# Kernel optimization log

Hardware: AMD Instinct MI355X
Metric: run time of the kernel (lower is better)

Reference implementation:

```python
import jax, jax.numpy as jnp
import numpy as np

B, S, D, H, DH, L, FF = 1, 4096, 768, 12, 64, 12, 3072
V, P = 50265, 4098
BLK = 256          # block size for banded attention
W_ONE = 256        # one-sided window (attention_window=512)
EPS = 1e-5


def layernorm(x, g, b):
    mu = jnp.mean(x, axis=-1, keepdims=True)
    var = jnp.mean((x - mu) ** 2, axis=-1, keepdims=True)
    return (x - mu) * jax.lax.rsqrt(var + EPS) * g + b


def sliding_attn(q, k, v, mask):
    # q,k,v: [B,H,S,DH]; mask: [B,S] (1=keep). Band |i-j| <= W_ONE.
    nb = S // BLK
    scale = 1.0 / np.sqrt(DH)
    qb = (q * scale).reshape(B, H, nb, BLK, DH)
    kp = jnp.pad(k, ((0, 0), (0, 0), (BLK, BLK), (0, 0))).reshape(B, H, nb + 2, BLK, DH)
    vp = jnp.pad(v, ((0, 0), (0, 0), (BLK, BLK), (0, 0))).reshape(B, H, nb + 2, BLK, DH)
    # each query block attends to key blocks [b-1, b, b+1] -> 3*BLK keys
    kb = jnp.concatenate([kp[:, :, :-2], kp[:, :, 1:-1], kp[:, :, 2:]], axis=3)
    vb = jnp.concatenate([vp[:, :, :-2], vp[:, :, 1:-1], vp[:, :, 2:]], axis=3)
    scores = jnp.einsum('bhnqd,bhnkd->bhnqk', qb, kb)  # [B,H,nb,BLK,3BLK]
    p = jnp.arange(BLK)[:, None]
    o = jnp.arange(3 * BLK)[None, :]
    rel = o - BLK - p
    band = (rel >= -W_ONE) & (rel <= W_ONE)            # [BLK,3BLK]
    mp = jnp.pad(mask.astype(bool), ((0, 0), (BLK, BLK))).reshape(B, nb + 2, BLK)
    mb = jnp.concatenate([mp[:, :-2], mp[:, 1:-1], mp[:, 2:]], axis=2)  # [B,nb,3BLK]
    valid = band[None, None, None, :, :] & mb[:, None, :, None, :]
    scores = jnp.where(valid, scores, jnp.asarray(-1e9, scores.dtype))
    probs = jax.nn.softmax(scores, axis=-1)
    out = jnp.einsum('bhnqk,bhnkd->bhnqd', probs, vb)
    return out.reshape(B, H, S, DH)


def setup_inputs() -> dict:
    keys = iter(jax.random.split(jax.random.key(0), 64))
    rn = lambda shape, s=0.02: jax.random.normal(next(keys), shape, jnp.float32) * s
    inp = {
        'input_ids': jax.random.randint(next(keys), (B, S), 0, V, jnp.int32),
        'attention_mask': jnp.ones((B, S), jnp.int32),
        'emb_word': rn((V, D)), 'emb_pos': rn((P, D)), 'emb_type': rn((1, D)),
        'emb_ln_g': jnp.ones((D,)), 'emb_ln_b': jnp.zeros((D,)),
        'Wq': rn((L, D, D)), 'bq': jnp.zeros((L, D)),
        'Wk': rn((L, D, D)), 'bk': jnp.zeros((L, D)),
        'Wv': rn((L, D, D)), 'bv': jnp.zeros((L, D)),
        'Wo': rn((L, D, D)), 'bo': jnp.zeros((L, D)),
        'ln1_g': jnp.ones((L, D)), 'ln1_b': jnp.zeros((L, D)),
        'W1': rn((L, D, FF)), 'b1': jnp.zeros((L, FF)),
        'W2': rn((L, FF, D)), 'b2': jnp.zeros((L, D)),
        'ln2_g': jnp.ones((L, D)), 'ln2_b': jnp.zeros((L, D)),
        'cW1': rn((D, 512)), 'cb1': jnp.zeros((512,)),
        'cW2': rn((512, 5)), 'cb2': jnp.zeros((5,)),
        'dW1': rn((D, 512)), 'db1': jnp.zeros((512,)),
        'dW2': rn((512, 10)), 'db2': jnp.zeros((10,)),
    }
    return inp


def reference(input_ids, attention_mask, emb_word, emb_pos, emb_type, emb_ln_g, emb_ln_b,
              Wq, bq, Wk, bk, Wv, bv, Wo, bo, ln1_g, ln1_b, W1, b1, W2, b2, ln2_g, ln2_b,
              cW1, cb1, cW2, cb2, dW1, db1, dW2, db2):
    mask = attention_mask
    # RoBERTa-style position ids (pad_token_id=1 offset)
    pos_ids = jnp.cumsum(mask, axis=1) * mask + 1
    x = emb_word[input_ids] + emb_pos[pos_ids] + emb_type[0]
    x = layernorm(x, emb_ln_g, emb_ln_b)
    for i in range(L):
        q = (x @ Wq[i] + bq[i]).reshape(B, S, H, DH).transpose(0, 2, 1, 3)
        k = (x @ Wk[i] + bk[i]).reshape(B, S, H, DH).transpose(0, 2, 1, 3)
        v = (x @ Wv[i] + bv[i]).reshape(B, S, H, DH).transpose(0, 2, 1, 3)
        a = sliding_attn(q, k, v, mask).transpose(0, 2, 1, 3).reshape(B, S, D)
        x = layernorm(x + a @ Wo[i] + bo[i], ln1_g[i], ln1_b[i])
        h = jax.nn.gelu(x @ W1[i] + b1[i], approximate=False)
        x = layernorm(x + h @ W2[i] + b2[i], ln2_g[i], ln2_b[i])
    pooled = x[:, 0, :]
    century = jax.nn.relu(pooled @ cW1 + cb1) @ cW2 + cb2
    decade = jax.nn.relu(pooled @ dW1 + db1) @ dW2 + db2
    return (century, decade)
```

## Files before the change

kernel.cpp:

```cpp
#include <hip/hip_runtime.h>
#include <hip/hip_bf16.h>
#include <math.h>

typedef __bf16 bf16_t;
typedef __bf16 bf16x8 __attribute__((ext_vector_type(8)));
typedef __bf16 bf16x4 __attribute__((ext_vector_type(4)));
typedef float  f32x4  __attribute__((ext_vector_type(4)));
typedef short  s16x4  __attribute__((ext_vector_type(4)));

#define S_LEN 4096
#define DMODEL 768
#define NHEAD 12
#define NLAYER 12
#define FFDIM 3072

static __device__ inline f32x4 mfma16x16x16(bf16x4 a, bf16x4 b, f32x4 c) {
#if __has_builtin(__builtin_amdgcn_mfma_f32_16x16x16_bf16)
  return __builtin_amdgcn_mfma_f32_16x16x16_bf16(a, b, c, 0, 0, 0);
#else
  return __builtin_amdgcn_mfma_f32_16x16x16bf16_1k(
      __builtin_bit_cast(s16x4, a), __builtin_bit_cast(s16x4, b), c, 0, 0, 0);
#endif
}

static __device__ inline void gload_lds16(const void* g, void* l) {
  __builtin_amdgcn_global_load_lds(
      (const __attribute__((address_space(1))) void*)g,
      (__attribute__((address_space(3))) void*)l, 16, 0, 0);
}

__global__ __launch_bounds__(256) void posid_kernel(const int* __restrict__ m,
                                                    int* __restrict__ pids) {
  __shared__ int ps[256];
  int t = threadIdx.x;
  int base = t * 16;
  int loc[16], mv[16];
  int s = 0;
#pragma unroll
  for (int j = 0; j < 16; ++j) { mv[j] = m[base + j]; s += mv[j]; loc[j] = s; }
  ps[t] = s;
  __syncthreads();
  for (int off = 1; off < 256; off <<= 1) {
    int v = (t >= off) ? ps[t - off] : 0;
    __syncthreads();
    ps[t] += v;
    __syncthreads();
  }
  int pre = t ? ps[t - 1] : 0;
#pragma unroll
  for (int j = 0; j < 16; ++j) pids[base + j] = (pre + loc[j]) * mv[j] + 1;
}

__device__ inline float blk_sum(float v, float* sred) {
#pragma unroll
  for (int o = 32; o; o >>= 1) v += __shfl_down(v, o, 64);
  int w = threadIdx.x >> 6;
  __syncthreads();
  if ((threadIdx.x & 63) == 0) sred[w] = v;
  __syncthreads();
  return sred[0] + sred[1] + sred[2] + sred[3];
}

__global__ __launch_bounds__(256) void embed_kernel(
    const int* __restrict__ ids, const int* __restrict__ pids,
    const float* __restrict__ ew, const float* __restrict__ ep,
    const float* __restrict__ et, const float* __restrict__ g,
    const float* __restrict__ b, float* __restrict__ xf,
    bf16_t* __restrict__ xb) {
  __shared__ float sred[4];
  int s = blockIdx.x, t = threadIdx.x;
  long wb = (long)ids[s] * DMODEL;
  long pb = (long)pids[s] * DMODEL;
  float v[3];
#pragma unroll
  for (int j = 0; j < 3; ++j) {
    int d = t + j * 256;
    v[j] = ew[wb + d] + ep[pb + d] + et[d];
  }
  float mu = blk_sum(v[0] + v[1] + v[2], sred) * (1.0f / 768.0f);
  float ss = 0.f;
#pragma unroll
  for (int j = 0; j < 3; ++j) { v[j] -= mu; ss += v[j] * v[j]; }
  float rs = rsqrtf(blk_sum(ss, sred) * (1.0f / 768.0f) + 1e-5f);
#pragma unroll
  for (int j = 0; j < 3; ++j) {
    int d = t + j * 256;
    float o = v[j] * rs * g[d] + b[d];
    xf[(long)s * DMODEL + d] = o;
    xb[(long)s * DMODEL + d] = (bf16_t)o;
  }
}

__global__ __launch_bounds__(256) void ln_kernel(
    const float* __restrict__ in, const float* __restrict__ g,
    const float* __restrict__ b, float* __restrict__ xf,
    bf16_t* __restrict__ xb) {
  __shared__ float sred[4];
  int row = blockIdx.x, t = threadIdx.x;
  const float* r = in + (long)row * DMODEL;
  float v[3] = {r[t], r[t + 256], r[t + 512]};
  float mu = blk_sum(v[0] + v[1] + v[2], sred) * (1.0f / 768.0f);
  float ss = 0.f;
#pragma unroll
  for (int j = 0; j < 3; ++j) { v[j] -= mu; ss += v[j] * v[j]; }
  float rs = rsqrtf(blk_sum(ss, sred) * (1.0f / 768.0f) + 1e-5f);
#pragma unroll
  for (int j = 0; j < 3; ++j) {
    int d = t + j * 256;
    float o = v[j] * rs * g[d] + b[d];
    xf[(long)row * DMODEL + d] = o;
    xb[(long)row * DMODEL + d] = (bf16_t)o;
  }
}

__global__ __launch_bounds__(256) void lnred_kernel(
    const float* __restrict__ pt, int ns, const float* __restrict__ gb,
    const float* __restrict__ g, const float* __restrict__ b,
    float* __restrict__ xf, bf16_t* __restrict__ xb) {
  __shared__ float sred[4];
  const long MN = (long)S_LEN * DMODEL;
  int row = blockIdx.x, t = threadIdx.x;
  long rb = (long)row * DMODEL;
  float v[3];
#pragma unroll
  for (int j = 0; j < 3; ++j) {
    int d = t + j * 256;
    float a = gb[d] + xf[rb + d];
    for (int z = 0; z < ns; ++z) a += pt[(long)z * MN + rb + d];
    v[j] = a;
  }
  float mu = blk_sum(v[0] + v[1] + v[2], sred) * (1.0f / 768.0f);
  float ss = 0.f;
#pragma unroll
  for (int j = 0; j < 3; ++j) { v[j] -= mu; ss += v[j] * v[j]; }
  float rs = rsqrtf(blk_sum(ss, sred) * (1.0f / 768.0f) + 1e-5f);
#pragma unroll
  for (int j = 0; j < 3; ++j) {
    int d = t + j * 256;
    float o = v[j] * rs * g[d] + b[d];
    xf[rb + d] = o;
    xb[rb + d] = (bf16_t)o;
  }
}

__global__ __launch_bounds__(256) void trc_kernel(const float* __restrict__ src,
                                                  bf16_t* __restrict__ dst,
                                                  int R, int C, long srcStride,
                                                  long dstStride) {
  src += (long)blockIdx.z * srcStride;
  dst += (long)blockIdx.z * dstStride;
  __shared__ float tile[64][65];
  int r0 = blockIdx.y * 64, c0 = blockIdx.x * 64;
  int t = threadIdx.x;
  int tr = t >> 4;
  int tc = (t & 15) * 4;
#pragma unroll
  for (int j = 0; j < 4; ++j) {
    int row = tr + j * 16;
    float4 v = *(const float4*)(src + (long)(r0 + row) * C + c0 + tc);
    tile[row][tc] = v.x; tile[row][tc + 1] = v.y;
    tile[row][tc + 2] = v.z; tile[row][tc + 3] = v.w;
  }
  __syncthreads();
#pragma unroll
  for (int j = 0; j < 4; ++j) {
    int row = tr + j * 16;
    bf16x4 v;
    v[0] = (bf16_t)tile[tc + 0][row]; v[1] = (bf16_t)tile[tc + 1][row];
    v[2] = (bf16_t)tile[tc + 2][row]; v[3] = (bf16_t)tile[tc + 3][row];
    *(bf16x4*)(dst + (long)(c0 + row) * R + r0 + tc) = v;
  }
}

__global__ __launch_bounds__(256) void tr_kernel(const bf16_t* __restrict__ src,
                                                 bf16_t* __restrict__ dst,
                                                 int R, int C) {
  __shared__ bf16_t tile[64][68];
  int r0 = blockIdx.y * 64, c0 = blockIdx.x * 64;
  int t = threadIdx.x;
  int tr = t >> 4;
  int tc = (t & 15) * 4;
#pragma unroll
  for (int j = 0; j < 4; ++j) {
    int row = tr + j * 16;
    bf16x4 v = *(const bf16x4*)(src + (long)(r0 + row) * C + c0 + tc);
    tile[row][tc] = v[0]; tile[row][tc + 1] = v[1];
    tile[row][tc + 2] = v[2]; tile[row][tc + 3] = v[3];
  }
  __syncthreads();
#pragma unroll
  for (int j = 0; j < 4; ++j) {
    int row = tr + j * 16;
    bf16x4 v;
    v[0] = tile[tc + 0][row]; v[1] = tile[tc + 1][row];
    v[2] = tile[tc + 2][row]; v[3] = tile[tc + 3][row];
    *(bf16x4*)(dst + (long)(c0 + row) * R + r0 + tc) = v;
  }
}

template <int EP>
__global__ __launch_bounds__(256) void gemm_kernel(
    const bf16_t* __restrict__ A, const bf16_t* __restrict__ Bt, long btStride,
    const float* b0, const float* b1, const float* b2,
    bf16_t* __restrict__ out, long outStride, const float* __restrict__ resf,
    float* __restrict__ tmp, int M, int N, int K, int kc) {
  int z = blockIdx.z;
  const float* bias = nullptr;
  int kBeg = 0;
  if constexpr (EP == 3) {
    kBeg = z * kc;
  } else {
    Bt += (long)z * btStride;
    bias = (z == 0) ? b0 : (z == 1 ? b1 : b2);
    out += (long)z * outStride;
  }

  int nwg = gridDim.x * gridDim.y;
  int bid = blockIdx.y * gridDim.x + blockIdx.x;
  int swz = (bid & 7) * (nwg >> 3) + (bid >> 3);
  int bx = swz % gridDim.x;
  int by = swz / gridDim.x;

  int tid = threadIdx.x;
  int lane = tid & 63;
  int wave = tid >> 6;
  int wm = (wave >> 1) * 64;
  int wn = (wave & 1) * 64;
  int l15 = lane & 15;
  int g4 = lane >> 4;
  int m0 = by * 128;
  int n0 = bx * 128;

  f32x4 acc[4][4] = {};

  __shared__ __align__(16) bf16_t As[128 * 64];
  __shared__ __align__(16) bf16_t Bs[128 * 64];

  for (int kt = kBeg; kt < kBeg + kc; kt += 64) {
#pragma unroll
    for (int c = 0; c < 4; ++c) {
      int L0 = c * 256 + wave * 64;
      int row = (L0 & 127) + lane;
      int gg = L0 >> 7;
      gload_lds16(A + (long)(m0 + row) * K + kt + gg * 8, As + L0 * 8);
      gload_lds16(Bt + (long)(n0 + row) * K + kt + gg * 8, Bs + L0 * 8);
    }
    __syncthreads();
#pragma unroll
    for (int ks = 0; ks < 2; ++ks) {
      bf16x8 af[4], bfr[4];
#pragma unroll
      for (int mt = 0; mt < 4; ++mt)
        af[mt] = *(const bf16x8*)(As + (((ks * 4 + g4) * 128) + wm + mt * 16 + l15) * 8);
#pragma unroll
      for (int nt = 0; nt < 4; ++nt)
        bfr[nt] = *(const bf16x8*)(Bs + (((ks * 4 + g4) * 128) + wn + nt * 16 + l15) * 8);
#pragma unroll
      for (int mt = 0; mt < 4; ++mt)
#pragma unroll
        for (int nt = 0; nt < 4; ++nt)
          acc[mt][nt] = __builtin_amdgcn_mfma_f32_16x16x32_bf16(
              af[mt], bfr[nt], acc[mt][nt], 0, 0, 0);
    }
    __syncthreads();
  }

#pragma unroll
  for (int mt = 0; mt < 4; ++mt)
#pragma unroll
    for (int nt = 0; nt < 4; ++nt) {
      int col = n0 + wn + nt * 16 + l15;
      float bval = (EP == 3) ? 0.f : bias[col];
#pragma unroll
      for (int r = 0; r < 4; ++r) {
        int row = m0 + wm + mt * 16 + g4 * 4 + r;
        float v = acc[mt][nt][r] + bval;
        if (EP == 0) {
          out[(long)row * N + col] = (bf16_t)v;
        } else if (EP == 1) {
          float ge = 0.5f * v * (1.0f + erff(v * 0.70710678118654752f));
          out[(long)row * N + col] = (bf16_t)ge;
        } else if (EP == 2) {
          tmp[(long)row * N + col] = v + resf[(long)row * N + col];
        } else {
          tmp[(long)z * ((long)M * N) + (long)row * N + col] = v;
        }
      }
    }
}

#define NEGM 30000.0f
__global__ __launch_bounds__(64) void attn_kernel(
    const bf16_t* __restrict__ q, const bf16_t* __restrict__ k,
    const bf16_t* __restrict__ vt, bf16_t* __restrict__ outb) {
  int qt = blockIdx.x * 32;
  int hcol = blockIdx.y * 64;
  int lane = threadIdx.x;
  int l15 = lane & 15, g4 = lane >> 4;
  __shared__ __align__(16) float sbuf[32];

  bf16x8 qf[2][2];
#pragma unroll
  for (int nt = 0; nt < 2; ++nt)
#pragma unroll
    for (int ks = 0; ks < 2; ++ks) {
      bf16x8 t = *(const bf16x8*)(q + (long)(qt + nt * 16 + l15) * DMODEL +
                                  hcol + ks * 32 + g4 * 8);
#pragma unroll
      for (int i = 0; i < 8; ++i) t[i] = (bf16_t)((float)t[i] * 0.125f);
      qf[nt][ks] = t;
    }

  f32x4 o[2][4] = {};
  float mS[2], lS[2];
#pragma unroll
  for (int nt = 0; nt < 2; ++nt) { mS[nt] = -NEGM; lS[nt] = 0.f; }

  int kstart = (qt >= 256) ? ((qt - 256) & ~63) : 0;
  int kend = (qt + 288 + 63) & ~63;
  if (kend > S_LEN) kend = S_LEN;

  for (int kb = kstart; kb < kend; kb += 64) {
    bf16x8 kf[4][2];
#pragma unroll
    for (int kt = 0; kt < 4; ++kt)
#pragma unroll
      for (int ks = 0; ks < 2; ++ks)
        kf[kt][ks] = *(const bf16x8*)(k + (long)(kb + kt * 16 + l15) * DMODEL +
                                      hcol + ks * 32 + g4 * 8);
    f32x4 st[4][2] = {};
#pragma unroll
    for (int kt = 0; kt < 4; ++kt)
#pragma unroll
      for (int nt = 0; nt < 2; ++nt) {
        st[kt][nt] = __builtin_amdgcn_mfma_f32_16x16x32_bf16(
            kf[kt][0], qf[nt][0], st[kt][nt], 0, 0, 0);
        st[kt][nt] = __builtin_amdgcn_mfma_f32_16x16x32_bf16(
            kf[kt][1], qf[nt][1], st[kt][nt], 0, 0, 0);
      }
    float alpha[2];
#pragma unroll
    for (int nt = 0; nt < 2; ++nt) {
      int qg = qt + nt * 16 + l15;
      float mx = -NEGM;
#pragma unroll
      for (int kt = 0; kt < 4; ++kt)
#pragma unroll
        for (int r = 0; r < 4; ++r) {
          int kg = kb + kt * 16 + g4 * 4 + r;
          bool valid = (kg >= qg - 256) && (kg <= qg + 256);
          float s = valid ? st[kt][nt][r] : -NEGM;
          st[kt][nt][r] = s;
          mx = fmaxf(mx, s);
        }
      mx = fmaxf(mx, __shfl_xor(mx, 16, 64));
      mx = fmaxf(mx, __shfl_xor(mx, 32, 64));
      float mnew = fmaxf(mS[nt], mx);
      alpha[nt] = exp2f((mS[nt] - mnew) * 1.44269504088896f);
      float ls = 0.f;
#pragma unroll
      for (int kt = 0; kt < 4; ++kt)
#pragma unroll
        for (int r = 0; r < 4; ++r) {
          float p = exp2f((st[kt][nt][r] - mnew) * 1.44269504088896f);
          st[kt][nt][r] = p;
          ls += p;
        }
      ls += __shfl_xor(ls, 16, 64);
      ls += __shfl_xor(ls, 32, 64);
      lS[nt] = lS[nt] * alpha[nt] + ls;
      mS[nt] = mnew;
    }
    if (g4 == 0) {
#pragma unroll
      for (int nt = 0; nt < 2; ++nt) sbuf[nt * 16 + l15] = alpha[nt];
    }
    __syncthreads();
    f32x4 av[2];
#pragma unroll
    for (int qmt = 0; qmt < 2; ++qmt)
      av[qmt] = *(const f32x4*)(sbuf + qmt * 16 + g4 * 4);
#pragma unroll
    for (int qmt = 0; qmt < 2; ++qmt)
#pragma unroll
      for (int dt = 0; dt < 4; ++dt)
#pragma unroll
        for (int r = 0; r < 4; ++r) o[qmt][dt][r] *= av[qmt][r];
#pragma unroll
    for (int kt = 0; kt < 4; ++kt) {
      bf16x4 pa[2];
#pragma unroll
      for (int qmt = 0; qmt < 2; ++qmt)
#pragma unroll
        for (int i = 0; i < 4; ++i) pa[qmt][i] = (bf16_t)st[kt][qmt][i];
      bf16x4 vf[4];
#pragma unroll
      for (int dt = 0; dt < 4; ++dt)
        vf[dt] = *(const bf16x4*)(vt + (long)(hcol + dt * 16 + l15) * S_LEN +
                                  kb + kt * 16 + g4 * 4);
#pragma unroll
      for (int qmt = 0; qmt < 2; ++qmt)
#pragma unroll
        for (int dt = 0; dt < 4; ++dt)
          o[qmt][dt] = mfma16x16x16(pa[qmt], vf[dt], o[qmt][dt]);
    }
    __syncthreads();
  }
  if (g4 == 0) {
#pragma unroll
    for (int nt = 0; nt < 2; ++nt) sbuf[nt * 16 + l15] = lS[nt];
  }
  __syncthreads();
  f32x4 lv[2];
#pragma unroll
  for (int qmt = 0; qmt < 2; ++qmt)
    lv[qmt] = *(const f32x4*)(sbuf + qmt * 16 + g4 * 4);
#pragma unroll
  for (int qmt = 0; qmt < 2; ++qmt)
#pragma unroll
    for (int dt = 0; dt < 4; ++dt)
#pragma unroll
      for (int r = 0; r < 4; ++r)
        outb[(long)(qt + qmt * 16 + g4 * 4 + r) * DMODEL + hcol + dt * 16 +
             l15] = (bf16_t)(o[qmt][dt][r] / lv[qmt][r]);
}

__global__ __launch_bounds__(256) void cls1_kernel(
    const float* __restrict__ xf, const float* cW1, const float* cb1,
    const float* dW1, const float* db1, float* __restrict__ hws) {
  __shared__ float red[4][64];
  bool dec = (blockIdx.y == 1);
  const float* W1 = dec ? dW1 : cW1;
  const float* B1 = dec ? db1 : cb1;
  float* h = hws + (dec ? 512 : 0);
  int t = threadIdx.x;
  int c = (t & 63) + blockIdx.x * 64;
  int ch = t >> 6;
  float s = 0.f;
  for (int k2 = ch * 192; k2 < ch * 192 + 192; ++k2)
    s += xf[k2] * W1[(long)k2 * 512 + c];
  red[ch][t & 63] = s;
  __syncthreads();
  if (t < 64) {
    int col = t + blockIdx.x * 64;
    float a = red[0][t] + red[1][t] + red[2][t] + red[3][t] + B1[col];
    h[col] = fmaxf(a, 0.f);
  }
}

__global__ __launch_bounds__(256) void cls2_kernel(
    const float* __restrict__ hws, const float* cW2, const float* cb2,
    const float* dW2, const float* db2, float* __restrict__ out) {
  __shared__ float sred[4];
  bool dec = (blockIdx.x == 1);
  const float* W2 = dec ? dW2 : cW2;
  const float* B2 = dec ? db2 : cb2;
  const float* h = hws + (dec ? 512 : 0);
  int nout = dec ? 10 : 5;
  float* op = out + (dec ? 5 : 0);
  int t = threadIdx.x;
  float h0 = h[t], h1 = h[t + 256];
  for (int o = 0; o < nout; ++o) {
    float s = h0 * W2[t * nout + o] + h1 * W2[(t + 256) * nout + o];
    float tot = blk_sum(s, sred);
    if (t == 0) op[o] = tot + B2[o];
    __syncthreads();
  }
}

extern "C" void kernel_launch(void* const* d_in, const int* in_sizes, int n_in,
                              void* d_out, int out_size, void* d_ws,
                              size_t ws_size, hipStream_t stream) {
  const int* ids = (const int*)d_in[0];
  const int* amask = (const int*)d_in[1];
  const float* emb_word = (const float*)d_in[2];
  const float* emb_pos = (const float*)d_in[3];
  const float* emb_type = (const float*)d_in[4];
  const float* emb_g = (const float*)d_in[5];
  const float* emb_b = (const float*)d_in[6];
  const float* Wq = (const float*)d_in[7];
  const float* bq = (const float*)d_in[8];
  const float* Wk = (const float*)d_in[9];
  const float* bk = (const float*)d_in[10];
  const float* Wv = (const float*)d_in[11];
  const float* bv = (const float*)d_in[12];
  const float* Wo = (const float*)d_in[13];
  const float* bo = (const float*)d_in[14];
  const float* ln1g = (const float*)d_in[15];
  const float* ln1b = (const float*)d_in[16];
  const float* W1 = (const float*)d_in[17];
  const float* b1 = (const float*)d_in[18];
  const float* W2 = (const float*)d_in[19];
  const float* b2 = (const float*)d_in[20];
  const float* ln2g = (const float*)d_in[21];
  const float* ln2b = (const float*)d_in[22];
  const float* cW1 = (const float*)d_in[23];
  const float* cb1 = (const float*)d_in[24];
  const float* cW2 = (const float*)d_in[25];
  const float* cb2 = (const float*)d_in[26];
  const float* dW1 = (const float*)d_in[27];
  const float* db1 = (const float*)d_in[28];
  const float* dW2 = (const float*)d_in[29];
  const float* db2 = (const float*)d_in[30];
  float* outp = (float*)d_out;

  const size_t SD = (size_t)S_LEN * DMODEL;
  const size_t DD = (size_t)DMODEL * DMODEL;
  const size_t DF = (size_t)DMODEL * FFDIM;
  const size_t SF = (size_t)S_LEN * FFDIM;

  char* p = (char*)d_ws;
  auto carve = [&](size_t bytes) {
    char* r = p;
    p += (bytes + 255) & ~(size_t)255;
    return (void*)r;
  };

  size_t actsBytes = SD * 2 + SD * 4 + 3 * SD * 2 + SD * 2 + SD * 2 + SF * 2 +
                     SD * 4 + S_LEN * 4 + 16 * 256;
  size_t fullW = (36 * DD + 12 * DD + 24 * DF) * 2 + 16 * 256;
  bool full = ws_size >= actsBytes + fullW;

  bf16_t *qkvt, *wot, *w1t, *w2t;
  if (full) {
    qkvt = (bf16_t*)carve(36 * DD * 2);
    wot = (bf16_t*)carve(12 * DD * 2);
    w1t = (bf16_t*)carve(12 * DF * 2);
    w2t = (bf16_t*)carve(12 * DF * 2);
  } else {
    qkvt = (bf16_t*)carve(3 * DD * 2);
    wot = (bf16_t*)carve(DD * 2);
    w1t = (bf16_t*)carve(DF * 2);
    w2t = (bf16_t*)carve(DF * 2);
  }
  bf16_t* xb = (bf16_t*)carve(SD * 2);
  float* xf = (float*)carve(SD * 4);
  bf16_t* qkv = (bf16_t*)carve(3 * SD * 2);
  bf16_t* vt = (bf16_t*)carve(SD * 2);
  bf16_t* attnb = (bf16_t*)carve(SD * 2);
  bf16_t* hbuf = (bf16_t*)carve(SF * 2);
  float* tmp = (float*)carve(SD * 4);
  int* pids = (int*)carve(S_LEN * 4);
  float* hws = (float*)carve(1024 * 4);
  float* ptmp = (float*)carve(4 * SD * 4);
  bool haveSplit = ((size_t)(p - (char*)d_ws) <= ws_size);

  posid_kernel<<<1, 256, 0, stream>>>(amask, pids);
  embed_kernel<<<S_LEN, 256, 0, stream>>>(ids, pids, emb_word, emb_pos,
                                          emb_type, emb_g, emb_b, xf, xb);

  if (full) {
    trc_kernel<<<dim3(12, 12, 12), 256, 0, stream>>>(Wq, qkvt, 768, 768, DD, 3 * DD);
    trc_kernel<<<dim3(12, 12, 12), 256, 0, stream>>>(Wk, qkvt + DD, 768, 768, DD, 3 * DD);
    trc_kernel<<<dim3(12, 12, 12), 256, 0, stream>>>(Wv, qkvt + 2 * DD, 768, 768, DD, 3 * DD);
    trc_kernel<<<dim3(12, 12, 12), 256, 0, stream>>>(Wo, wot, 768, 768, DD, DD);
    trc_kernel<<<dim3(48, 12, 12), 256, 0, stream>>>(W1, w1t, 768, 3072, DF, DF);
    trc_kernel<<<dim3(12, 48, 12), 256, 0, stream>>>(W2, w2t, 3072, 768, DF, DF);
  }

  for (int i = 0; i < NLAYER; ++i) {
    const bf16_t *qkvt_i, *wot_i, *w1t_i, *w2t_i;
    if (full) {
      qkvt_i = qkvt + (size_t)i * 3 * DD;
      wot_i = wot + (size_t)i * DD;
      w1t_i = w1t + (size_t)i * DF;
      w2t_i = w2t + (size_t)i * DF;
    } else {
      trc_kernel<<<dim3(12, 12, 1), 256, 0, stream>>>(Wq + (size_t)i * DD, qkvt, 768, 768, 0, 0);
      trc_kernel<<<dim3(12, 12, 1), 256, 0, stream>>>(Wk + (size_t)i * DD, qkvt + DD, 768, 768, 0, 0);
      trc_kernel<<<dim3(12, 12, 1), 256, 0, stream>>>(Wv + (size_t)i * DD, qkvt + 2 * DD, 768, 768, 0, 0);
      trc_kernel<<<dim3(12, 12, 1), 256, 0, stream>>>(Wo + (size_t)i * DD, wot, 768, 768, 0, 0);
      trc_kernel<<<dim3(48, 12, 1), 256, 0, stream>>>(W1 + (size_t)i * DF, w1t, 768, 3072, 0, 0);
      trc_kernel<<<dim3(12, 48, 1), 256, 0, stream>>>(W2 + (size_t)i * DF, w2t, 3072, 768, 0, 0);
      qkvt_i = qkvt; wot_i = wot; w1t_i = w1t; w2t_i = w2t;
    }
    gemm_kernel<0><<<dim3(6, 32, 3), 256, 0, stream>>>(
        xb, qkvt_i, (long)DD, bq + i * 768, bk + i * 768, bv + i * 768, qkv,
        (long)SD, nullptr, nullptr, S_LEN, 768, 768, 768);
    tr_kernel<<<dim3(12, 64, 1), 256, 0, stream>>>(qkv + 2 * SD, vt, 4096, 768);
    attn_kernel<<<dim3(128, 12), 64, 0, stream>>>(qkv, qkv + SD, vt, attnb);
    if (haveSplit) {
      gemm_kernel<3><<<dim3(6, 32, 2), 256, 0, stream>>>(
          attnb, wot_i, 0, nullptr, nullptr, nullptr, nullptr, 0, nullptr,
          ptmp, S_LEN, 768, 768, 384);
      lnred_kernel<<<S_LEN, 256, 0, stream>>>(ptmp, 2, bo + i * 768,
                                              ln1g + i * 768, ln1b + i * 768,
                                              xf, xb);
    } else {
      gemm_kernel<2><<<dim3(6, 32, 1), 256, 0, stream>>>(
          attnb, wot_i, 0, bo + i * 768, nullptr, nullptr, nullptr, 0, xf, tmp,
          S_LEN, 768, 768, 768);
      ln_kernel<<<S_LEN, 256, 0, stream>>>(tmp, ln1g + i * 768, ln1b + i * 768,
                                           xf, xb);
    }
    gemm_kernel<1><<<dim3(24, 32, 1), 256, 0, stream>>>(
        xb, w1t_i, 0, b1 + (size_t)i * FFDIM, nullptr, nullptr, hbuf, 0,
        nullptr, nullptr, S_LEN, FFDIM, 768, 768);
    if (haveSplit) {
      gemm_kernel<3><<<dim3(6, 32, 4), 256, 0, stream>>>(
          hbuf, w2t_i, 0, nullptr, nullptr, nullptr, nullptr, 0, nullptr,
          ptmp, S_LEN, 768, 3072, 768);
      lnred_kernel<<<S_LEN, 256, 0, stream>>>(ptmp, 4, b2 + i * 768,
                                              ln2g + i * 768, ln2b + i * 768,
                                              xf, xb);
    } else {
      gemm_kernel<2><<<dim3(6, 32, 1), 256, 0, stream>>>(
          hbuf, w2t_i, 0, b2 + i * 768, nullptr, nullptr, nullptr, 0, xf, tmp,
          S_LEN, 768, 3072, 3072);
      ln_kernel<<<S_LEN, 256, 0, stream>>>(tmp, ln2g + i * 768, ln2b + i * 768,
                                           xf, xb);
    }
  }
  cls1_kernel<<<dim3(8, 2), 256, 0, stream>>>(xf, cW1, cb1, dW1, db1, hws);
  cls2_kernel<<<2, 256, 0, stream>>>(hws, cW2, cb2, dW2, db2, outp);
}
```

Measured before the change: 3.596 ms.

## Prefetch next K tile in registers and replace LDS alpha broadcast with shuffles

The attention kernel now loads the next K tile into registers while softmax and PV of the current tile run, and issues all V loads at the top of each iteration instead of inside the PV loop. The shared-memory broadcast of alpha and l, along with its __syncthreads barriers, is replaced by cross-lane __shfl. s_setprio hints are placed around the MFMA sections. This targets memory latency and barrier stalls in the attention loop, at the cost of more live registers, which may lower occupancy.

```diff
diff --git a/kernel.cpp b/kernel.cpp
--- a/kernel.cpp
+++ b/kernel.cpp
@@ -297,7 +297,6 @@
   int hcol = blockIdx.y * 64;
   int lane = threadIdx.x;
   int l15 = lane & 15, g4 = lane >> 4;
-  __shared__ __align__(16) float sbuf[32];
 
   bf16x8 qf[2][2];
 #pragma unroll
@@ -320,15 +319,25 @@
   int kend = (qt + 288 + 63) & ~63;
   if (kend > S_LEN) kend = S_LEN;
 
+  bf16x8 kf[4][2];
+#pragma unroll
+  for (int kt = 0; kt < 4; ++kt)
+#pragma unroll
+    for (int ks = 0; ks < 2; ++ks)
+      kf[kt][ks] = *(const bf16x8*)(k + (long)(kstart + kt * 16 + l15) * DMODEL +
+                                    hcol + ks * 32 + g4 * 8);
+
   for (int kb = kstart; kb < kend; kb += 64) {
-    bf16x8 kf[4][2];
+    bf16x4 vf[4][4];
 #pragma unroll
     for (int kt = 0; kt < 4; ++kt)
 #pragma unroll
-      for (int ks = 0; ks < 2; ++ks)
-        kf[kt][ks] = *(const bf16x8*)(k + (long)(kb + kt * 16 + l15) * DMODEL +
-                                      hcol + ks * 32 + g4 * 8);
+      for (int dt = 0; dt < 4; ++dt)
+        vf[kt][dt] = *(const bf16x4*)(vt + (long)(hcol + dt * 16 + l15) * S_LEN +
+                                      kb + kt * 16 + g4 * 4);
+
     f32x4 st[4][2] = {};
+    __builtin_amdgcn_s_setprio(1);
 #pragma unroll
     for (int kt = 0; kt < 4; ++kt)
 #pragma unroll
@@ -338,6 +347,19 @@
         st[kt][nt] = __builtin_amdgcn_mfma_f32_16x16x32_bf16(
             kf[kt][1], qf[nt][1], st[kt][nt], 0, 0, 0);
       }
+    __builtin_amdgcn_s_setprio(0);
+
+    int kbn = kb + 64;
+    bf16x8 kfn[4][2];
+    if (kbn < kend) {
+#pragma unroll
+      for (int kt = 0; kt < 4; ++kt)
+#pragma unroll
+        for (int ks = 0; ks < 2; ++ks)
+          kfn[kt][ks] = *(const bf16x8*)(k + (long)(kbn + kt * 16 + l15) * DMODEL +
+                                         hcol + ks * 32 + g4 * 8);
+    }
+
     float alpha[2];
 #pragma unroll
     for (int nt = 0; nt < 2; ++nt) {
@@ -371,21 +393,19 @@
       lS[nt] = lS[nt] * alpha[nt] + ls;
       mS[nt] = mnew;
     }
-    if (g4 == 0) {
-#pragma unroll
-      for (int nt = 0; nt < 2; ++nt) sbuf[nt * 16 + l15] = alpha[nt];
-    }
-    __syncthreads();
     f32x4 av[2];
 #pragma unroll
     for (int qmt = 0; qmt < 2; ++qmt)
-      av[qmt] = *(const f32x4*)(sbuf + qmt * 16 + g4 * 4);
+#pragma unroll
+      for (int r = 0; r < 4; ++r)
+        av[qmt][r] = __shfl(alpha[qmt], g4 * 4 + r, 64);
 #pragma unroll
     for (int qmt = 0; qmt < 2; ++qmt)
 #pragma unroll
       for (int dt = 0; dt < 4; ++dt)
 #pragma unroll
         for (int r = 0; r < 4; ++r) o[qmt][dt][r] *= av[qmt][r];
+    __builtin_amdgcn_s_setprio(1);
 #pragma unroll
     for (int kt = 0; kt < 4; ++kt) {
       bf16x4 pa[2];
@@ -393,28 +413,26 @@
       for (int qmt = 0; qmt < 2; ++qmt)
 #pragma unroll
         for (int i = 0; i < 4; ++i) pa[qmt][i] = (bf16_t)st[kt][qmt][i];
-      bf16x4 vf[4];
-#pragma unroll
-      for (int dt = 0; dt < 4; ++dt)
-        vf[dt] = *(const bf16x4*)(vt + (long)(hcol + dt * 16 + l15) * S_LEN +
-                                  kb + kt * 16 + g4 * 4);
 #pragma unroll
       for (int qmt = 0; qmt < 2; ++qmt)
 #pragma unroll
         for (int dt = 0; dt < 4; ++dt)
-          o[qmt][dt] = mfma16x16x16(pa[qmt], vf[dt], o[qmt][dt]);
-    }
-    __syncthreads();
-  }
-  if (g4 == 0) {
-#pragma unroll
-    for (int nt = 0; nt < 2; ++nt) sbuf[nt * 16 + l15] = lS[nt];
-  }
-  __syncthreads();
+          o[qmt][dt] = mfma16x16x16(pa[qmt], vf[kt][dt], o[qmt][dt]);
+    }
+    __builtin_amdgcn_s_setprio(0);
+    if (kbn < kend) {
+#pragma unroll
+      for (int kt = 0; kt < 4; ++kt)
+#pragma unroll
+        for (int ks = 0; ks < 2; ++ks) kf[kt][ks] = kfn[kt][ks];
+    }
+  }
   f32x4 lv[2];
 #pragma unroll
   for (int qmt = 0; qmt < 2; ++qmt)
-    lv[qmt] = *(const f32x4*)(sbuf + qmt * 16 + g4 * 4);
+#pragma unroll
+    for (int r = 0; r < 4; ++r)
+      lv[qmt][r] = __shfl(lS[qmt], g4 * 4 + r, 64);
 #pragma unroll
   for (int qmt = 0; qmt < 2; ++qmt)
 #pragma unroll
```

Result: no change. 3.580 ms (-0.5%).
